# Optimization experiments

Measured on AMD Instinct MI355X. Metric: run time of the kernel, lower is better.

Reference implementation:

```python
import jax, jax.numpy as jnp
import numpy as np

HEAD = 8
EMB = 512
D_K = EMB // HEAD


def setup_inputs() -> dict:
    key = jax.random.key(0)
    ks = jax.random.split(key, 12)
    B, S = 2, 2048
    scale = 1.0 / np.sqrt(EMB)
    inp = {
        "query": jax.random.normal(ks[0], (B, S, EMB), jnp.float32),
        "key": jax.random.normal(ks[1], (B, S, EMB), jnp.float32),
        "value": jax.random.normal(ks[2], (B, S, EMB), jnp.float32),
        # subsequentMask(size): lower-triangular causal mask, shape [1, S, S]
        "mask": jnp.tril(jnp.ones((1, S, S), jnp.int32)),
        "Wq": jax.random.normal(ks[3], (EMB, EMB), jnp.float32) * scale,
        "bq": jnp.zeros((EMB,), jnp.float32),
        "Wk": jax.random.normal(ks[4], (EMB, EMB), jnp.float32) * scale,
        "bk": jnp.zeros((EMB,), jnp.float32),
        "Wv": jax.random.normal(ks[5], (EMB, EMB), jnp.float32) * scale,
        "bv": jnp.zeros((EMB,), jnp.float32),
        "Wo": jax.random.normal(ks[6], (EMB, EMB), jnp.float32) * scale,
        "bo": jnp.zeros((EMB,), jnp.float32),
    }
    return inp


def _split_heads(x, B):
    # [B, S, E] -> [B, H, S, d_k]
    return x.reshape(B, -1, HEAD, D_K).transpose(0, 2, 1, 3)


def reference(query, key, value, mask, Wq, bq, Wk, bk, Wv, bv, Wo, bo):
    B, S, _ = query.shape
    # linear projections (x @ W^T + b, torch nn.Linear convention)
    q = _split_heads(query @ Wq.T + bq, B)
    k = _split_heads(key @ Wk.T + bk, B)
    v = _split_heads(value @ Wv.T + bv, B)
    # scaled dot-product attention; scores [B, H, S, S]
    scores = jnp.einsum('bhqd,bhkd->bhqk', q, k) / jnp.sqrt(jnp.float32(D_K))
    # mask [1,S,S] -> unsqueeze(0) -> [1,1,S,S]; masked_fill(mask==0, -1e9)
    m = mask[None, ...]  # [1, 1, S, S]
    scores = jnp.where(m == 0, jnp.float32(-1e9), scores)
    p_attn = jax.nn.softmax(scores, axis=-1)
    # dropout is identity at inference (deterministic reference)
    x = jnp.einsum('bhqk,bhkd->bhqd', p_attn, v)
    x = x.transpose(0, 2, 1, 3).reshape(B, S, EMB)
    return x @ Wo.T + bo
```

## Files before the change

kernel.cpp:

```cpp
#include <hip/hip_runtime.h>
#include <hip/hip_bf16.h>


#define SEQ 2048
#define EMB 512
#define NH  8
#define DKD 64

typedef __bf16 bf16x8 __attribute__((ext_vector_type(8)));
typedef float  f32x4  __attribute__((ext_vector_type(4)));
typedef _Float16 f16x8 __attribute__((ext_vector_type(8)));

__device__ __forceinline__ ushort f2bf(float f) {
  unsigned x = __float_as_uint(f);
  return (ushort)((x + 0x7fffu + ((x >> 16) & 1u)) >> 16);
}
__device__ __forceinline__ unsigned pkbf(float a, float b) {
  __hip_bfloat162 h = __float22bfloat162_rn(make_float2(a, b));
  unsigned u;
  __builtin_memcpy(&u, &h, 4);
  return u;
}

__device__ __forceinline__ void cp16(const ushort* g, ushort* l) {
  __builtin_amdgcn_global_load_lds(
      (const __attribute__((address_space(1))) void*)g,
      (__attribute__((address_space(3))) void*)l, 16, 0, 0);
}

__global__ __launch_bounds__(256) void cvt7(
    const float* s0, const float* s1, const float* s2, const float* s3,
    const float* s4, const float* s5, const float* s6,
    ushort* d0, ushort* d1, ushort* d2, ushort* d3,
    ushort* d4, ushort* d5, ushort* d6) {
  const float* src; ushort* dst; int n;
  switch (blockIdx.y) {
    case 0: src = s0; dst = d0; n = 2 * SEQ * EMB; break;
    case 1: src = s1; dst = d1; n = 2 * SEQ * EMB; break;
    case 2: src = s2; dst = d2; n = 2 * SEQ * EMB; break;
    case 3: src = s3; dst = d3; n = EMB * EMB;     break;
    case 4: src = s4; dst = d4; n = EMB * EMB;     break;
    case 5: src = s5; dst = d5; n = EMB * EMB;     break;
    default: src = s6; dst = d6; n = EMB * EMB;    break;
  }
  int i = (blockIdx.x * 256 + threadIdx.x) * 8;
  if (i >= n) return;
  float4 a = *reinterpret_cast<const float4*>(src + i);
  float4 b = *reinterpret_cast<const float4*>(src + i + 4);
  uint4 t = make_uint4(pkbf(a.x, a.y), pkbf(a.z, a.w),
                       pkbf(b.x, b.y), pkbf(b.z, b.w));
  *reinterpret_cast<uint4*>(dst + i) = t;
}

__device__ __forceinline__ void gemm_body(const ushort* __restrict__ X,
                                          const ushort* __restrict__ W,
                                          const float* __restrict__ bias,
                                          void* __restrict__ C,
                                          int wg, int mode, bool of32,
                                          float oscale,
                                          ushort* sA, ushort* sB) {
  const int N = EMB, K = EMB;
  const int tid = threadIdx.x;
  const int w = tid >> 6, lane = tid & 63, r16 = lane & 15, g = lane >> 4;
  const int nT = N / 64;
  const int m0 = (wg / nT) * 128;
  const int n0 = (wg % nT) * 64;
  const int wm = w * 32;

  f32x4 acc[2][4] = {};

  auto stage = [&](int buf, int k0) {
#pragma unroll
    for (int i = 0; i < 2; ++i) {
      const int s = i * 256 + w * 64 + lane;
      const int row = s >> 2;
      const int col = (s & 3) ^ ((row >> 1) & 3);
      cp16(X + (size_t)(m0 + row) * K + k0 + col * 8, sA + buf * 4096 + s * 8);
    }
    {
      const int s = w * 64 + lane;
      const int row = s >> 2;
      const int col = (s & 3) ^ ((row >> 1) & 3);
      cp16(W + (size_t)(n0 + row) * K + k0 + col * 8, sB + buf * 2048 + s * 8);
    }
  };

  stage(0, 0);
  const int NIT = K / 32;
  for (int it = 0; it < NIT; ++it) {
    const int cur = it & 1;
    __syncthreads();
    if (it + 1 < NIT) stage(cur ^ 1, (it + 1) * 32);

    const ushort* bA = sA + cur * 4096;
    const ushort* bB = sB + cur * 2048;
    bf16x8 af[2], bfr[4];
#pragma unroll
    for (int f = 0; f < 2; ++f) {
      const int row = wm + f * 16 + r16;
      af[f] = *reinterpret_cast<const bf16x8*>(bA + row * 32 + ((g ^ ((row >> 1) & 3)) << 3));
    }
#pragma unroll
    for (int t = 0; t < 4; ++t) {
      const int row = t * 16 + r16;
      bfr[t] = *reinterpret_cast<const bf16x8*>(bB + row * 32 + ((g ^ ((row >> 1) & 3)) << 3));
    }
#pragma unroll
    for (int f = 0; f < 2; ++f)
#pragma unroll
      for (int t = 0; t < 4; ++t)
        acc[f][t] = __builtin_amdgcn_mfma_f32_16x16x32_bf16(af[f], bfr[t], acc[f][t], 0, 0, 0);
  }

#pragma unroll
  for (int t = 0; t < 4; ++t) {
    const int n = n0 + t * 16 + r16;
    const float bv = bias[n];
#pragma unroll
    for (int f = 0; f < 2; ++f) {
#pragma unroll
      for (int r = 0; r < 4; ++r) {
        const int m = m0 + wm + f * 16 + g * 4 + r;
        const float v = (acc[f][t][r] + bv) * oscale;
        size_t addr;
        if (mode == 0) {
          addr = (size_t)m * N + n;
        } else {
          const int b = m >> 11, s = m & (SEQ - 1);
          const int h = n >> 6, dk = n & (DKD - 1);
          addr = (mode == 1) ? (((size_t)(b * NH + h) * SEQ + s) * DKD + dk)
                             : (((size_t)(b * NH + h) * DKD + dk) * SEQ + s);
        }
        if (of32) ((float*)C)[addr] = v;
        else      ((ushort*)C)[addr] = f2bf(v);
      }
    }
  }
}

__global__ __launch_bounds__(256) void proj_qkv(
    const ushort* Xq, const ushort* Xk, const ushort* Xv,
    const ushort* Wq, const ushort* Wk, const ushort* Wv,
    const float* bq, const float* bk, const float* bv,
    ushort* Qo, ushort* Ko, ushort* Vo) {
  __shared__ __align__(16) ushort sA[2 * 128 * 32];
  __shared__ __align__(16) ushort sB[2 * 64 * 32];
  const int z = blockIdx.z;
  const ushort* X = (z == 0) ? Xq : (z == 1) ? Xk : Xv;
  const ushort* W = (z == 0) ? Wq : (z == 1) ? Wk : Wv;
  const float* bias = (z == 0) ? bq : (z == 1) ? bk : bv;
  ushort* C = (z == 0) ? Qo : (z == 1) ? Ko : Vo;
  const int h = blockIdx.x;
  const int wg = (h & 7) * 32 + (h >> 3);
  gemm_body(X, W, bias, C, wg, (z == 2) ? 2 : 1, false,
            (z == 0) ? 0.18033688011112042f : 1.0f, sA, sB);
}

__global__ __launch_bounds__(256) void out_proj(const ushort* X, const ushort* W,
                                                const float* bias, float* C) {
  __shared__ __align__(16) ushort sA[2 * 128 * 32];
  __shared__ __align__(16) ushort sB[2 * 64 * 32];
  const int h = blockIdx.x;
  const int wg = (h & 7) * 32 + (h >> 3);
  gemm_body(X, W, bias, C, wg, 0, true, 1.0f, sA, sB);
}

__global__ __launch_bounds__(256) void flash_attn(const ushort* __restrict__ Q,
                                                  const ushort* __restrict__ Kb,
                                                  const ushort* __restrict__ Vt,
                                                  _Float16* __restrict__ O0,
                                                  _Float16* __restrict__ O1,
                                                  _Float16* __restrict__ O2,
                                                  float* __restrict__ P0,
                                                  float* __restrict__ P1,
                                                  float* __restrict__ P2) {
  __shared__ __align__(16) ushort sK[64 * 64];
  __shared__ __align__(16) ushort sV[64 * 64];
  __shared__ __align__(16) ushort sP[4][16 * 64];

  const int tid = threadIdx.x, w = tid >> 6, lane = tid & 63;
  const int r16 = lane & 15, g = lane >> 4;
  const int hwid = blockIdx.x;
  const int xcd = hwid & 7;
  const int j   = hwid >> 3;
  const int bh  = xcd * 2 + (j & 1);
  const int qb  = 31 - ((j >> 1) & 31);
  const int sp  = j >> 6;
  const int tiles = qb + 1;
  const int kt0 = (tiles * sp) / 3;
  const int kt1 = (tiles * (sp + 1)) / 3;

  const int q0 = qb * 64 + w * 16;
  const int q  = q0 + r16;

  const ushort* qp = Q + ((size_t)bh * SEQ + q0 + r16) * DKD + g * 8;
  const bf16x8 qf0 = *reinterpret_cast<const bf16x8*>(qp);
  const bf16x8 qf1 = *reinterpret_cast<const bf16x8*>(qp + 32);

  f32x4 oacc[4] = {};
  float psum = 0.f;

  const ushort* kbase = Kb + (size_t)bh * SEQ * DKD;
  const ushort* vbase = Vt + (size_t)bh * DKD * SEQ;

  auto stageKV = [&](int kb) {
#pragma unroll
    for (int i = 0; i < 2; ++i) {
      const int s = i * 256 + w * 64 + lane;
      const int row = s >> 3;
      const int col = (s & 7) ^ (row & 7);
      cp16(kbase + (size_t)(kb + row) * DKD + col * 8, &sK[(size_t)(i * 256 + w * 64) * 8]);
      cp16(vbase + (size_t)row * SEQ + kb + col * 8,   &sV[(size_t)(i * 256 + w * 64) * 8]);
    }
  };

  for (int kt = kt0; kt < kt1; ++kt) {
    const int kb = kt * 64;
    __syncthreads();
    stageKV(kb);
    __syncthreads();

    f32x4 sc[4] = {};
#pragma unroll
    for (int t = 0; t < 4; ++t) {
      const int row = t * 16 + r16;
      const bf16x8 a0 = *reinterpret_cast<const bf16x8*>(&sK[row * 64 + (((0 + g) ^ (row & 7)) << 3)]);
      const bf16x8 a1 = *reinterpret_cast<const bf16x8*>(&sK[row * 64 + (((4 + g) ^ (row & 7)) << 3)]);
      sc[t] = __builtin_amdgcn_mfma_f32_16x16x32_bf16(a0, qf0, sc[t], 0, 0, 0);
      sc[t] = __builtin_amdgcn_mfma_f32_16x16x32_bf16(a1, qf1, sc[t], 0, 0, 0);
    }

    const bool diag = (kb + 63) > q0;
    float p[16];
#pragma unroll
    for (int t = 0; t < 4; ++t)
#pragma unroll
      for (int r = 0; r < 4; ++r) {
        float e = __builtin_amdgcn_exp2f(sc[t][r]);
        if (diag && (kb + t * 16 + g * 4 + r) > q) e = 0.f;
        p[t * 4 + r] = e;
      }
    float s0 = (p[0] + p[1]) + (p[2] + p[3]);
    float s1 = (p[4] + p[5]) + (p[6] + p[7]);
    float s2 = (p[8] + p[9]) + (p[10] + p[11]);
    float s3 = (p[12] + p[13]) + (p[14] + p[15]);
    psum += (s0 + s1) + (s2 + s3);

#pragma unroll
    for (int t = 0; t < 4; ++t) {
      const unsigned lo = pkbf(p[t * 4],     p[t * 4 + 1]);
      const unsigned hi = pkbf(p[t * 4 + 2], p[t * 4 + 3]);
      const int key0 = t * 16 + g * 4;
      const int slot = (key0 >> 3) ^ (r16 & 7);
      *reinterpret_cast<uint2*>(&sP[w][r16 * 64 + slot * 8 + (key0 & 7)]) = make_uint2(lo, hi);
    }
    __asm__ volatile("s_waitcnt lgkmcnt(0)" ::: "memory");

    const bf16x8 pf0 = *reinterpret_cast<const bf16x8*>(&sP[w][r16 * 64 + (((0 + g) ^ (r16 & 7)) << 3)]);
    const bf16x8 pf1 = *reinterpret_cast<const bf16x8*>(&sP[w][r16 * 64 + (((4 + g) ^ (r16 & 7)) << 3)]);
#pragma unroll
    for (int t = 0; t < 4; ++t) {
      const int row = t * 16 + r16;
      const bf16x8 b0 = *reinterpret_cast<const bf16x8*>(&sV[row * 64 + (((0 + g) ^ (row & 7)) << 3)]);
      const bf16x8 b1 = *reinterpret_cast<const bf16x8*>(&sV[row * 64 + (((4 + g) ^ (row & 7)) << 3)]);
      oacc[t] = __builtin_amdgcn_mfma_f32_16x16x32_bf16(pf0, b0, oacc[t], 0, 0, 0);
      oacc[t] = __builtin_amdgcn_mfma_f32_16x16x32_bf16(pf1, b1, oacc[t], 0, 0, 0);
    }
  }

  psum += __shfl_xor(psum, 16);
  psum += __shfl_xor(psum, 32);
  float* Pc = (sp == 0) ? P0 : (sp == 1) ? P1 : P2;
  _Float16* Oc = (sp == 0) ? O0 : (sp == 1) ? O1 : O2;
  if (g == 0) Pc[(size_t)bh * SEQ + q0 + r16] = psum;
#pragma unroll
  for (int r = 0; r < 4; ++r) {
    const int mq = q0 + g * 4 + r;
#pragma unroll
    for (int t = 0; t < 4; ++t)
      Oc[((size_t)bh * SEQ + mq) * DKD + t * 16 + r16] = (_Float16)oacc[t][r];
  }
}

__global__ __launch_bounds__(256) void attn_norm(const _Float16* __restrict__ O0,
                                                 const _Float16* __restrict__ O1,
                                                 const _Float16* __restrict__ O2,
                                                 const float* __restrict__ P0,
                                                 const float* __restrict__ P1,
                                                 const float* __restrict__ P2,
                                                 ushort* __restrict__ Ab) {
  const int idx = blockIdx.x * 256 + threadIdx.x;
  const int d0 = (idx & 7) * 8;
  const int s  = (idx >> 3) & (SEQ - 1);
  const int bh = idx >> 14;
  const size_t o = ((size_t)bh * SEQ + s) * DKD + d0;
  const f16x8 a = *reinterpret_cast<const f16x8*>(O0 + o);
  const f16x8 b = *reinterpret_cast<const f16x8*>(O1 + o);
  const f16x8 c = *reinterpret_cast<const f16x8*>(O2 + o);
  const size_t ps = (size_t)bh * SEQ + s;
  const float inv = 1.0f / (P0[ps] + P1[ps] + P2[ps]);
  float r[8];
#pragma unroll
  for (int i = 0; i < 8; ++i)
    r[i] = ((float)a[i] + (float)b[i] + (float)c[i]) * inv;
  uint4 t = make_uint4(pkbf(r[0], r[1]), pkbf(r[2], r[3]),
                       pkbf(r[4], r[5]), pkbf(r[6], r[7]));
  const int bb = bh >> 3, hh = bh & 7;
  *reinterpret_cast<uint4*>(Ab + ((size_t)bb * SEQ + s) * EMB + hh * DKD + d0) = t;
}

extern "C" void kernel_launch(void* const* d_in, const int* in_sizes, int n_in,
                              void* d_out, int out_size, void* d_ws, size_t ws_size,
                              hipStream_t stream) {
  const float* q_in = (const float*)d_in[0];
  const float* k_in = (const float*)d_in[1];
  const float* v_in = (const float*)d_in[2];
  const float* Wq = (const float*)d_in[4];
  const float* bq = (const float*)d_in[5];
  const float* Wk = (const float*)d_in[6];
  const float* bk = (const float*)d_in[7];
  const float* Wv = (const float*)d_in[8];
  const float* bv = (const float*)d_in[9];
  const float* Wo = (const float*)d_in[10];
  const float* bo = (const float*)d_in[11];
  float* out = (float*)d_out;
  ushort* ws = (ushort*)d_ws;

  const size_t NX = (size_t)2 * SEQ * EMB;
  const size_t NW = (size_t)EMB * EMB;
  const size_t NO = (size_t)2 * NH * SEQ * DKD;
  ushort* Xq = ws;
  ushort* Xk = Xq + NX;
  ushort* Xv = Xk + NX;
  ushort* WqB = Xv + NX;
  ushort* WkB = WqB + NW;
  ushort* WvB = WkB + NW;
  ushort* WoB = WvB + NW;
  ushort* Qb  = WoB + NW;
  ushort* Kbf = Qb + NX;
  ushort* Vbf = Kbf + NX;
  ushort* Ab  = Vbf + NX;
  _Float16* O0 = (_Float16*)(Ab + NX);
  _Float16* O1 = O0 + NO;
  _Float16* O2 = O1 + NO;
  float*  P0  = (float*)(O2 + NO);
  float*  P1  = P0 + (size_t)2 * NH * SEQ;
  float*  P2  = P1 + (size_t)2 * NH * SEQ;

  dim3 blk(256);
  cvt7<<<dim3(1024, 7), blk, 0, stream>>>(q_in, k_in, v_in, Wq, Wk, Wv, Wo,
                                          Xq, Xk, Xv, WqB, WkB, WvB, WoB);
  proj_qkv<<<dim3((2 * SEQ / 128) * (EMB / 64), 1, 3), blk, 0, stream>>>(
      Xq, Xk, Xv, WqB, WkB, WvB, bq, bk, bv, Qb, Kbf, Vbf);
  flash_attn<<<dim3(512 * 3), blk, 0, stream>>>(Qb, Kbf, Vbf, O0, O1, O2, P0, P1, P2);
  attn_norm<<<dim3(1024), blk, 0, stream>>>(O0, O1, O2, P0, P1, P2, Ab);
  out_proj<<<dim3((2 * SEQ / 128) * (EMB / 64)), blk, 0, stream>>>(Ab, WoB, bo, out);
}
```

Baseline: 154.4 us.

## Fuse split-K attention normalization into output projection and register-prefetch KV tiles

Removes the separate attn_norm kernel: the output projection GEMM now reads the three fp16 partial attention outputs and row sums directly, combines and normalizes them in registers, and writes bf16 tiles into shared memory. This drops one launch and a round trip of the intermediate A buffer. Flash attention replaces async global-to-LDS copies with a register prefetch of the next K/V tile, overlapping loads with compute, and adds an occupancy hint of 6 blocks. The fused GEMM re-reads the partials once per column tile (8x redundant) and uses more registers.

```diff
diff --git a/kernel.cpp b/kernel.cpp
--- a/kernel.cpp
+++ b/kernel.cpp
@@ -56,7 +56,7 @@
                                           const ushort* __restrict__ W,
                                           const float* __restrict__ bias,
                                           void* __restrict__ C,
-                                          int wg, int mode, bool of32,
+                                          int wg, int mode,
                                           float oscale,
                                           ushort* sA, ushort* sB) {
   const int N = EMB, K = EMB;
@@ -122,17 +122,12 @@
       for (int r = 0; r < 4; ++r) {
         const int m = m0 + wm + f * 16 + g * 4 + r;
         const float v = (acc[f][t][r] + bv) * oscale;
-        size_t addr;
-        if (mode == 0) {
-          addr = (size_t)m * N + n;
-        } else {
-          const int b = m >> 11, s = m & (SEQ - 1);
-          const int h = n >> 6, dk = n & (DKD - 1);
-          addr = (mode == 1) ? (((size_t)(b * NH + h) * SEQ + s) * DKD + dk)
-                             : (((size_t)(b * NH + h) * DKD + dk) * SEQ + s);
-        }
-        if (of32) ((float*)C)[addr] = v;
-        else      ((ushort*)C)[addr] = f2bf(v);
+        const int b = m >> 11, s = m & (SEQ - 1);
+        const int h = n >> 6, dk = n & (DKD - 1);
+        const size_t addr =
+            (mode == 1) ? (((size_t)(b * NH + h) * SEQ + s) * DKD + dk)
+                        : (((size_t)(b * NH + h) * DKD + dk) * SEQ + s);
+        ((ushort*)C)[addr] = f2bf(v);
       }
     }
   }
@@ -152,28 +147,134 @@
   ushort* C = (z == 0) ? Qo : (z == 1) ? Ko : Vo;
   const int h = blockIdx.x;
   const int wg = (h & 7) * 32 + (h >> 3);
-  gemm_body(X, W, bias, C, wg, (z == 2) ? 2 : 1, false,
+  gemm_body(X, W, bias, C, wg, (z == 2) ? 2 : 1,
             (z == 0) ? 0.18033688011112042f : 1.0f, sA, sB);
 }
 
-__global__ __launch_bounds__(256) void out_proj(const ushort* X, const ushort* W,
-                                                const float* bias, float* C) {
+__global__ __launch_bounds__(256) void out_proj_fused(
+    const _Float16* __restrict__ O0, const _Float16* __restrict__ O1,
+    const _Float16* __restrict__ O2, const float* __restrict__ P0,
+    const float* __restrict__ P1, const float* __restrict__ P2,
+    const ushort* __restrict__ W, const float* __restrict__ bias,
+    float* __restrict__ C) {
   __shared__ __align__(16) ushort sA[2 * 128 * 32];
   __shared__ __align__(16) ushort sB[2 * 64 * 32];
-  const int h = blockIdx.x;
-  const int wg = (h & 7) * 32 + (h >> 3);
-  gemm_body(X, W, bias, C, wg, 0, true, 1.0f, sA, sB);
-}
-
-__global__ __launch_bounds__(256) void flash_attn(const ushort* __restrict__ Q,
-                                                  const ushort* __restrict__ Kb,
-                                                  const ushort* __restrict__ Vt,
-                                                  _Float16* __restrict__ O0,
-                                                  _Float16* __restrict__ O1,
-                                                  _Float16* __restrict__ O2,
-                                                  float* __restrict__ P0,
-                                                  float* __restrict__ P1,
-                                                  float* __restrict__ P2) {
+  const int tid = threadIdx.x;
+  const int w = tid >> 6, lane = tid & 63, r16 = lane & 15, g = lane >> 4;
+  const int hb = blockIdx.x;
+  const int wg = (hb & 7) * 32 + (hb >> 3);
+  const int m0 = (wg >> 3) * 128;
+  const int n0 = (wg & 7) * 64;
+  const int wm = w * 32;
+  const int b = m0 >> 11;
+  const int srow0 = m0 & (SEQ - 1);
+
+  f32x4 acc[2][4] = {};
+
+  int arow[2], acol[2];
+#pragma unroll
+  for (int i = 0; i < 2; ++i) {
+    const int s = i * 256 + tid;
+    arow[i] = s >> 2;
+    acol[i] = (s & 3) ^ ((arow[i] >> 1) & 3);
+  }
+
+  uint4 ra[2][3];
+  float rpsum[2];
+  auto regloadA = [&](int it) {
+    const int hh = it >> 1;
+    const size_t bhb = (size_t)b * NH + hh;
+#pragma unroll
+    for (int i = 0; i < 2; ++i) {
+      const int dk = (it * 32 + acol[i] * 8) & (DKD - 1);
+      const size_t ps = bhb * SEQ + srow0 + arow[i];
+      const size_t off = ps * DKD + dk;
+      ra[i][0] = *reinterpret_cast<const uint4*>(O0 + off);
+      ra[i][1] = *reinterpret_cast<const uint4*>(O1 + off);
+      ra[i][2] = *reinterpret_cast<const uint4*>(O2 + off);
+      rpsum[i] = P0[ps] + P1[ps] + P2[ps];
+    }
+  };
+  auto writeA = [&](int buf) {
+#pragma unroll
+    for (int i = 0; i < 2; ++i) {
+      const int s = i * 256 + tid;
+      f16x8 va, vb, vc;
+      __builtin_memcpy(&va, &ra[i][0], 16);
+      __builtin_memcpy(&vb, &ra[i][1], 16);
+      __builtin_memcpy(&vc, &ra[i][2], 16);
+      const float inv = 1.0f / rpsum[i];
+      float r[8];
+#pragma unroll
+      for (int j = 0; j < 8; ++j)
+        r[j] = ((float)va[j] + (float)vb[j] + (float)vc[j]) * inv;
+      uint4 t = make_uint4(pkbf(r[0], r[1]), pkbf(r[2], r[3]),
+                           pkbf(r[4], r[5]), pkbf(r[6], r[7]));
+      *reinterpret_cast<uint4*>(sA + buf * 4096 + s * 8) = t;
+    }
+  };
+  auto stageB = [&](int buf, int k0) {
+    const int s = w * 64 + lane;
+    const int row = s >> 2;
+    const int col = (s & 3) ^ ((row >> 1) & 3);
+    cp16(W + (size_t)(n0 + row) * EMB + k0 + col * 8, sB + buf * 2048 + s * 8);
+  };
+
+  regloadA(0);
+  stageB(0, 0);
+  writeA(0);
+  regloadA(1);
+  const int NIT = EMB / 32;
+  for (int it = 0; it < NIT; ++it) {
+    const int cur = it & 1;
+    __syncthreads();
+    if (it + 1 < NIT) stageB(cur ^ 1, (it + 1) * 32);
+
+    const ushort* bA = sA + cur * 4096;
+    const ushort* bB = sB + cur * 2048;
+    bf16x8 af[2], bfr[4];
+#pragma unroll
+    for (int f = 0; f < 2; ++f) {
+      const int row = wm + f * 16 + r16;
+      af[f] = *reinterpret_cast<const bf16x8*>(bA + row * 32 + ((g ^ ((row >> 1) & 3)) << 3));
+    }
+#pragma unroll
+    for (int t = 0; t < 4; ++t) {
+      const int row = t * 16 + r16;
+      bfr[t] = *reinterpret_cast<const bf16x8*>(bB + row * 32 + ((g ^ ((row >> 1) & 3)) << 3));
+    }
+#pragma unroll
+    for (int f = 0; f < 2; ++f)
+#pragma unroll
+      for (int t = 0; t < 4; ++t)
+        acc[f][t] = __builtin_amdgcn_mfma_f32_16x16x32_bf16(af[f], bfr[t], acc[f][t], 0, 0, 0);
+
+    if (it + 1 < NIT) {
+      writeA(cur ^ 1);
+      if (it + 2 < NIT) regloadA(it + 2);
+    }
+  }
+
+#pragma unroll
+  for (int t = 0; t < 4; ++t) {
+    const int n = n0 + t * 16 + r16;
+    const float bv = bias[n];
+#pragma unroll
+    for (int f = 0; f < 2; ++f)
+#pragma unroll
+      for (int r = 0; r < 4; ++r) {
+        const int m = m0 + wm + f * 16 + g * 4 + r;
+        C[(size_t)m * EMB + n] = acc[f][t][r] + bv;
+      }
+  }
+}
+
+__global__ __launch_bounds__(256, 6) void flash_attn(
+    const ushort* __restrict__ Q, const ushort* __restrict__ Kb,
+    const ushort* __restrict__ Vt,
+    _Float16* __restrict__ O0, _Float16* __restrict__ O1,
+    _Float16* __restrict__ O2,
+    float* __restrict__ P0, float* __restrict__ P1, float* __restrict__ P2) {
   __shared__ __align__(16) ushort sK[64 * 64];
   __shared__ __align__(16) ushort sV[64 * 64];
   __shared__ __align__(16) ushort sP[4][16 * 64];
@@ -203,22 +304,30 @@
   const ushort* kbase = Kb + (size_t)bh * SEQ * DKD;
   const ushort* vbase = Vt + (size_t)bh * DKD * SEQ;
 
-  auto stageKV = [&](int kb) {
+  uint4 rk[2], rv[2];
+  auto regload = [&](int kb) {
 #pragma unroll
     for (int i = 0; i < 2; ++i) {
       const int s = i * 256 + w * 64 + lane;
       const int row = s >> 3;
       const int col = (s & 7) ^ (row & 7);
-      cp16(kbase + (size_t)(kb + row) * DKD + col * 8, &sK[(size_t)(i * 256 + w * 64) * 8]);
-      cp16(vbase + (size_t)row * SEQ + kb + col * 8,   &sV[(size_t)(i * 256 + w * 64) * 8]);
+      rk[i] = *reinterpret_cast<const uint4*>(kbase + (size_t)(kb + row) * DKD + col * 8);
+      rv[i] = *reinterpret_cast<const uint4*>(vbase + (size_t)row * SEQ + kb + col * 8);
     }
   };
 
+  if (kt0 < kt1) regload(kt0 * 64);
   for (int kt = kt0; kt < kt1; ++kt) {
     const int kb = kt * 64;
     __syncthreads();
-    stageKV(kb);
+#pragma unroll
+    for (int i = 0; i < 2; ++i) {
+      const int s = i * 256 + w * 64 + lane;
+      *reinterpret_cast<uint4*>(&sK[(size_t)s * 8]) = rk[i];
+      *reinterpret_cast<uint4*>(&sV[(size_t)s * 8]) = rv[i];
+    }
     __syncthreads();
+    if (kt + 1 < kt1) regload((kt + 1) * 64);
 
     f32x4 sc[4] = {};
 #pragma unroll
@@ -280,33 +389,6 @@
     for (int t = 0; t < 4; ++t)
       Oc[((size_t)bh * SEQ + mq) * DKD + t * 16 + r16] = (_Float16)oacc[t][r];
   }
-}
-
-__global__ __launch_bounds__(256) void attn_norm(const _Float16* __restrict__ O0,
-                                                 const _Float16* __restrict__ O1,
-                                                 const _Float16* __restrict__ O2,
-                                                 const float* __restrict__ P0,
-                                                 const float* __restrict__ P1,
-                                                 const float* __restrict__ P2,
-                                                 ushort* __restrict__ Ab) {
-  const int idx = blockIdx.x * 256 + threadIdx.x;
-  const int d0 = (idx & 7) * 8;
-  const int s  = (idx >> 3) & (SEQ - 1);
-  const int bh = idx >> 14;
-  const size_t o = ((size_t)bh * SEQ + s) * DKD + d0;
-  const f16x8 a = *reinterpret_cast<const f16x8*>(O0 + o);
-  const f16x8 b = *reinterpret_cast<const f16x8*>(O1 + o);
-  const f16x8 c = *reinterpret_cast<const f16x8*>(O2 + o);
-  const size_t ps = (size_t)bh * SEQ + s;
-  const float inv = 1.0f / (P0[ps] + P1[ps] + P2[ps]);
-  float r[8];
-#pragma unroll
-  for (int i = 0; i < 8; ++i)
-    r[i] = ((float)a[i] + (float)b[i] + (float)c[i]) * inv;
-  uint4 t = make_uint4(pkbf(r[0], r[1]), pkbf(r[2], r[3]),
-                       pkbf(r[4], r[5]), pkbf(r[6], r[7]));
-  const int bb = bh >> 3, hh = bh & 7;
-  *reinterpret_cast<uint4*>(Ab + ((size_t)bb * SEQ + s) * EMB + hh * DKD + d0) = t;
 }
 
 extern "C" void kernel_launch(void* const* d_in, const int* in_sizes, int n_in,
@@ -339,8 +421,7 @@
   ushort* Qb  = WoB + NW;
   ushort* Kbf = Qb + NX;
   ushort* Vbf = Kbf + NX;
-  ushort* Ab  = Vbf + NX;
-  _Float16* O0 = (_Float16*)(Ab + NX);
+  _Float16* O0 = (_Float16*)(Vbf + NX);
   _Float16* O1 = O0 + NO;
   _Float16* O2 = O1 + NO;
   float*  P0  = (float*)(O2 + NO);
@@ -353,6 +434,6 @@
   proj_qkv<<<dim3((2 * SEQ / 128) * (EMB / 64), 1, 3), blk, 0, stream>>>(
       Xq, Xk, Xv, WqB, WkB, WvB, bq, bk, bv, Qb, Kbf, Vbf);
   flash_attn<<<dim3(512 * 3), blk, 0, stream>>>(Qb, Kbf, Vbf, O0, O1, O2, P0, P1, P2);
-  attn_norm<<<dim3(1024), blk, 0, stream>>>(O0, O1, O2, P0, P1, P2, Ab);
-  out_proj<<<dim3((2 * SEQ / 128) * (EMB / 64)), blk, 0, stream>>>(Ab, WoB, bo, out);
-}
+  out_proj_fused<<<dim3((2 * SEQ / 128) * (EMB / 64)), blk, 0, stream>>>(
+      O0, O1, O2, P0, P1, P2, WoB, bo, out);
+}
```

Result: slower. 200.2 us (+29.7%).

## Split causal attention KV range adaptively per query block for load balance

Applied to the files above, without the earlier changes.

Replaces the fixed three-way split of each query block's KV range with a variable split count ns = ceil((qb+1)/7), so long causal rows get up to five partial blocks and short rows get one. The grid shrinks from 1536 to 1440 blocks, each doing roughly seven KV tiles, which evens out per-block work. The normalization kernel then sums only the partials that exist for each row. This needs two extra partial O/P buffers and a small serial loop at block start to decode the block index.

```diff
diff --git a/kernel.cpp b/kernel.cpp
--- a/kernel.cpp
+++ b/kernel.cpp
@@ -165,15 +165,14 @@
   gemm_body(X, W, bias, C, wg, 0, true, 1.0f, sA, sB);
 }
 
-__global__ __launch_bounds__(256) void flash_attn(const ushort* __restrict__ Q,
-                                                  const ushort* __restrict__ Kb,
-                                                  const ushort* __restrict__ Vt,
-                                                  _Float16* __restrict__ O0,
-                                                  _Float16* __restrict__ O1,
-                                                  _Float16* __restrict__ O2,
-                                                  float* __restrict__ P0,
-                                                  float* __restrict__ P1,
-                                                  float* __restrict__ P2) {
+__global__ __launch_bounds__(256) void flash_attn(
+    const ushort* __restrict__ Q, const ushort* __restrict__ Kb,
+    const ushort* __restrict__ Vt,
+    _Float16* __restrict__ O0, _Float16* __restrict__ O1,
+    _Float16* __restrict__ O2, _Float16* __restrict__ O3,
+    _Float16* __restrict__ O4,
+    float* __restrict__ P0, float* __restrict__ P1, float* __restrict__ P2,
+    float* __restrict__ P3, float* __restrict__ P4) {
   __shared__ __align__(16) ushort sK[64 * 64];
   __shared__ __align__(16) ushort sV[64 * 64];
   __shared__ __align__(16) ushort sP[4][16 * 64];
@@ -182,13 +181,20 @@
   const int r16 = lane & 15, g = lane >> 4;
   const int hwid = blockIdx.x;
   const int xcd = hwid & 7;
-  const int j   = hwid >> 3;
-  const int bh  = xcd * 2 + (j & 1);
-  const int qb  = 31 - ((j >> 1) & 31);
-  const int sp  = j >> 6;
+  const int i   = hwid >> 3;
+  const int bh  = xcd * 2 + (i & 1);
+  int rem = i >> 1;
+  int qb = 31;
+  int ns;
+  for (;; --qb) {
+    ns = (qb + 7) / 7;
+    if (rem < ns) break;
+    rem -= ns;
+  }
+  const int slot = rem;
   const int tiles = qb + 1;
-  const int kt0 = (tiles * sp) / 3;
-  const int kt1 = (tiles * (sp + 1)) / 3;
+  const int kt0 = (tiles * slot) / ns;
+  const int kt1 = (tiles * (slot + 1)) / ns;
 
   const int q0 = qb * 64 + w * 16;
   const int q  = q0 + r16;
@@ -205,12 +211,12 @@
 
   auto stageKV = [&](int kb) {
 #pragma unroll
-    for (int i = 0; i < 2; ++i) {
-      const int s = i * 256 + w * 64 + lane;
+    for (int ii = 0; ii < 2; ++ii) {
+      const int s = ii * 256 + w * 64 + lane;
       const int row = s >> 3;
       const int col = (s & 7) ^ (row & 7);
-      cp16(kbase + (size_t)(kb + row) * DKD + col * 8, &sK[(size_t)(i * 256 + w * 64) * 8]);
-      cp16(vbase + (size_t)row * SEQ + kb + col * 8,   &sV[(size_t)(i * 256 + w * 64) * 8]);
+      cp16(kbase + (size_t)(kb + row) * DKD + col * 8, &sK[(size_t)(ii * 256 + w * 64) * 8]);
+      cp16(vbase + (size_t)row * SEQ + kb + col * 8,   &sV[(size_t)(ii * 256 + w * 64) * 8]);
     }
   };
 
@@ -251,8 +257,8 @@
       const unsigned lo = pkbf(p[t * 4],     p[t * 4 + 1]);
       const unsigned hi = pkbf(p[t * 4 + 2], p[t * 4 + 3]);
       const int key0 = t * 16 + g * 4;
-      const int slot = (key0 >> 3) ^ (r16 & 7);
-      *reinterpret_cast<uint2*>(&sP[w][r16 * 64 + slot * 8 + (key0 & 7)]) = make_uint2(lo, hi);
+      const int slt = (key0 >> 3) ^ (r16 & 7);
+      *reinterpret_cast<uint2*>(&sP[w][r16 * 64 + slt * 8 + (key0 & 7)]) = make_uint2(lo, hi);
     }
     __asm__ volatile("s_waitcnt lgkmcnt(0)" ::: "memory");
 
@@ -270,8 +276,10 @@
 
   psum += __shfl_xor(psum, 16);
   psum += __shfl_xor(psum, 32);
-  float* Pc = (sp == 0) ? P0 : (sp == 1) ? P1 : P2;
-  _Float16* Oc = (sp == 0) ? O0 : (sp == 1) ? O1 : O2;
+  float* Pc = (slot == 0) ? P0 : (slot == 1) ? P1 : (slot == 2) ? P2
+            : (slot == 3) ? P3 : P4;
+  _Float16* Oc = (slot == 0) ? O0 : (slot == 1) ? O1 : (slot == 2) ? O2
+               : (slot == 3) ? O3 : O4;
   if (g == 0) Pc[(size_t)bh * SEQ + q0 + r16] = psum;
 #pragma unroll
   for (int r = 0; r < 4; ++r) {
@@ -282,27 +290,55 @@
   }
 }
 
-__global__ __launch_bounds__(256) void attn_norm(const _Float16* __restrict__ O0,
-                                                 const _Float16* __restrict__ O1,
-                                                 const _Float16* __restrict__ O2,
-                                                 const float* __restrict__ P0,
-                                                 const float* __restrict__ P1,
-                                                 const float* __restrict__ P2,
-                                                 ushort* __restrict__ Ab) {
+__global__ __launch_bounds__(256) void attn_norm(
+    const _Float16* __restrict__ O0, const _Float16* __restrict__ O1,
+    const _Float16* __restrict__ O2, const _Float16* __restrict__ O3,
+    const _Float16* __restrict__ O4,
+    const float* __restrict__ P0, const float* __restrict__ P1,
+    const float* __restrict__ P2, const float* __restrict__ P3,
+    const float* __restrict__ P4, ushort* __restrict__ Ab) {
   const int idx = blockIdx.x * 256 + threadIdx.x;
   const int d0 = (idx & 7) * 8;
   const int s  = (idx >> 3) & (SEQ - 1);
   const int bh = idx >> 14;
+  const int qb = s >> 6;
+  const int ns = (qb + 7) / 7;
   const size_t o = ((size_t)bh * SEQ + s) * DKD + d0;
-  const f16x8 a = *reinterpret_cast<const f16x8*>(O0 + o);
-  const f16x8 b = *reinterpret_cast<const f16x8*>(O1 + o);
-  const f16x8 c = *reinterpret_cast<const f16x8*>(O2 + o);
   const size_t ps = (size_t)bh * SEQ + s;
-  const float inv = 1.0f / (P0[ps] + P1[ps] + P2[ps]);
   float r[8];
-#pragma unroll
-  for (int i = 0; i < 8; ++i)
-    r[i] = ((float)a[i] + (float)b[i] + (float)c[i]) * inv;
+  {
+    const f16x8 a = *reinterpret_cast<const f16x8*>(O0 + o);
+#pragma unroll
+    for (int k = 0; k < 8; ++k) r[k] = (float)a[k];
+  }
+  float pden = P0[ps];
+  if (ns > 1) {
+    const f16x8 a = *reinterpret_cast<const f16x8*>(O1 + o);
+#pragma unroll
+    for (int k = 0; k < 8; ++k) r[k] += (float)a[k];
+    pden += P1[ps];
+  }
+  if (ns > 2) {
+    const f16x8 a = *reinterpret_cast<const f16x8*>(O2 + o);
+#pragma unroll
+    for (int k = 0; k < 8; ++k) r[k] += (float)a[k];
+    pden += P2[ps];
+  }
+  if (ns > 3) {
+    const f16x8 a = *reinterpret_cast<const f16x8*>(O3 + o);
+#pragma unroll
+    for (int k = 0; k < 8; ++k) r[k] += (float)a[k];
+    pden += P3[ps];
+  }
+  if (ns > 4) {
+    const f16x8 a = *reinterpret_cast<const f16x8*>(O4 + o);
+#pragma unroll
+    for (int k = 0; k < 8; ++k) r[k] += (float)a[k];
+    pden += P4[ps];
+  }
+  const float inv = 1.0f / pden;
+#pragma unroll
+  for (int k = 0; k < 8; ++k) r[k] *= inv;
   uint4 t = make_uint4(pkbf(r[0], r[1]), pkbf(r[2], r[3]),
                        pkbf(r[4], r[5]), pkbf(r[6], r[7]));
   const int bb = bh >> 3, hh = bh & 7;
@@ -343,16 +379,23 @@
   _Float16* O0 = (_Float16*)(Ab + NX);
   _Float16* O1 = O0 + NO;
   _Float16* O2 = O1 + NO;
-  float*  P0  = (float*)(O2 + NO);
+  _Float16* O3 = O2 + NO;
+  _Float16* O4 = O3 + NO;
+  float*  P0  = (float*)(O4 + NO);
   float*  P1  = P0 + (size_t)2 * NH * SEQ;
   float*  P2  = P1 + (size_t)2 * NH * SEQ;
+  float*  P3  = P2 + (size_t)2 * NH * SEQ;
+  float*  P4  = P3 + (size_t)2 * NH * SEQ;
 
   dim3 blk(256);
   cvt7<<<dim3(1024, 7), blk, 0, stream>>>(q_in, k_in, v_in, Wq, Wk, Wv, Wo,
                                           Xq, Xk, Xv, WqB, WkB, WvB, WoB);
   proj_qkv<<<dim3((2 * SEQ / 128) * (EMB / 64), 1, 3), blk, 0, stream>>>(
       Xq, Xk, Xv, WqB, WkB, WvB, bq, bk, bv, Qb, Kbf, Vbf);
-  flash_attn<<<dim3(512 * 3), blk, 0, stream>>>(Qb, Kbf, Vbf, O0, O1, O2, P0, P1, P2);
-  attn_norm<<<dim3(1024), blk, 0, stream>>>(O0, O1, O2, P0, P1, P2, Ab);
+  flash_attn<<<dim3(1440), blk, 0, stream>>>(Qb, Kbf, Vbf,
+                                             O0, O1, O2, O3, O4,
+                                             P0, P1, P2, P3, P4);
+  attn_norm<<<dim3(1024), blk, 0, stream>>>(O0, O1, O2, O3, O4,
+                                            P0, P1, P2, P3, P4, Ab);
   out_proj<<<dim3((2 * SEQ / 128) * (EMB / 64)), blk, 0, stream>>>(Ab, WoB, bo, out);
 }
```

New measurement: 157.4 us. No clear change (+2.0%).
